# Performance work log

Hardware: AMD Instinct MI355X
Metric: run time of the kernel (lower is better)

## Reference

```python
import jax, jax.numpy as jnp
import numpy as np

DIM = 512
HEADS = 16
WS = 8          # window size
SHIFT = 4       # shift size
POSMLP = 32
MLP_HID = 4 * DIM
B = 32
HH = 56
WW = 56
EPS = 1e-5


def setup_inputs() -> dict:
    key = jax.random.key(0)
    ks = jax.random.split(key, 20)
    s = 0.02
    inp = {
        'x': jax.random.normal(ks[0], (B, HH * WW, DIM), jnp.float32),
        'g1': jnp.ones((DIM,), jnp.float32),
        'be1': jnp.zeros((DIM,), jnp.float32),
        'w_qkv': s * jax.random.normal(ks[1], (3 * DIM, DIM), jnp.float32),
        'b_qkv': jnp.zeros((3 * DIM,), jnp.float32),
        'pm_w1': s * jax.random.normal(ks[2], (POSMLP, 2), jnp.float32),
        'pm_b1': jnp.zeros((POSMLP,), jnp.float32),
        'pm_w2': s * jax.random.normal(ks[3], (HEADS, POSMLP), jnp.float32),
        'pm_b2': jnp.zeros((HEADS,), jnp.float32),
        'w_proj': s * jax.random.normal(ks[4], (DIM, DIM), jnp.float32),
        'b_proj': jnp.zeros((DIM,), jnp.float32),
        'g2': jnp.ones((DIM,), jnp.float32),
        'be2': jnp.zeros((DIM,), jnp.float32),
        'w_fc1': s * jax.random.normal(ks[5], (MLP_HID, DIM), jnp.float32),
        'b_fc1': jnp.zeros((MLP_HID,), jnp.float32),
        'w_fc2': s * jax.random.normal(ks[6], (DIM, MLP_HID), jnp.float32),
        'b_fc2': jnp.zeros((DIM,), jnp.float32),
        'H': HH,
        'W': WW,
    }
    return inp


def _layernorm(x, g, b):
    m = jnp.mean(x, -1, keepdims=True)
    v = jnp.mean(jnp.square(x - m), -1, keepdims=True)
    return (x - m) * jax.lax.rsqrt(v + EPS) * g + b


def _shift_mask(H, W, ws, sh):
    # static numpy construction of the (nW, N, N) 0/-100 shift mask
    img = np.zeros((H, W), np.float32)
    cnt = 0
    for hs in (slice(0, -ws), slice(-ws, -sh), slice(-sh, None)):
        for wsl in (slice(0, -ws), slice(-ws, -sh), slice(-sh, None)):
            img[hs, wsl] = cnt
            cnt += 1
    mw = img.reshape(H // ws, ws, W // ws, ws).transpose(0, 2, 1, 3).reshape(-1, ws * ws)
    diff = mw[:, None, :] - mw[:, :, None]
    return jnp.asarray(np.where(diff != 0, -100.0, 0.0).astype(np.float32))


def _pos_bias(ws, pm_w1, pm_b1, pm_w2, pm_b2):
    # log-CPB relative position bias computed by a tiny MLP -> (heads, N, N)
    g = jnp.stack(jnp.meshgrid(jnp.arange(ws), jnp.arange(ws), indexing='ij'))
    coords = g.reshape(2, -1).astype(jnp.float32)        # [2, N]
    d = coords[:, :, None] - coords[:, None, :]          # [2, N, N]
    d = jnp.sign(d) * jnp.log1p(jnp.abs(d))
    h = jax.nn.relu(jnp.einsum('cnm,oc->onm', d, pm_w1) + pm_b1[:, None, None])
    return jnp.einsum('onm,ho->hnm', h, pm_w2) + pm_b2[:, None, None]


def reference(x, g1, be1, w_qkv, b_qkv, pm_w1, pm_b1, pm_w2, pm_b2,
              w_proj, b_proj, g2, be2, w_fc1, b_fc1, w_fc2, b_fc2, H, W):
    ws, sh, nh = WS, SHIFT, HEADS
    Bb, L, C = x.shape
    hd = C // nh
    scale = hd ** -0.5
    N = ws * ws
    nWh, nWw = H // ws, W // ws
    nW = nWh * nWw

    shortcut = x
    xn = _layernorm(x, g1, be1).reshape(Bb, H, W, C)
    xn = jnp.roll(xn, (-sh, -sh), axis=(1, 2))
    # window partition -> (B*nW, N, C)
    xw = xn.reshape(Bb, nWh, ws, nWw, ws, C).transpose(0, 1, 3, 2, 4, 5).reshape(-1, N, C)

    qkv = (xw @ w_qkv.T + b_qkv).reshape(-1, N, 3, nh, hd).transpose(2, 0, 3, 1, 4)
    q, k, v = qkv[0], qkv[1], qkv[2]           # each (B*nW, nh, N, hd)

    attn = jnp.einsum('bhnd,bhmd->bhnm', q * scale, k)
    attn = attn + _pos_bias(ws, pm_w1, pm_b1, pm_w2, pm_b2)[None]

    mask = _shift_mask(H, W, ws, sh)           # (nW, N, N)
    attn = attn.reshape(Bb, nW, nh, N, N) + mask[None, :, None]
    attn = jax.nn.softmax(attn.reshape(-1, nh, N, N), axis=-1)

    out = jnp.einsum('bhnm,bhmd->bhnd', attn, v).transpose(0, 2, 1, 3).reshape(-1, N, C)
    out = out @ w_proj.T + b_proj

    # window reverse + roll back
    out = out.reshape(Bb, nWh, nWw, ws, ws, C).transpose(0, 1, 3, 2, 4, 5).reshape(Bb, H, W, C)
    out = jnp.roll(out, (sh, sh), axis=(1, 2)).reshape(Bb, L, C)

    x1 = shortcut + out
    h = jax.nn.gelu(_layernorm(x1, g2, be2) @ w_fc1.T + b_fc1, approximate=False)
    return x1 + (h @ w_fc2.T + b_fc2)
```

## Files before the change

kernel.cpp:

```cpp
#include <hip/hip_runtime.h>
#include <math.h>

typedef __bf16 bf16;
typedef bf16 bf16x8 __attribute__((ext_vector_type(8)));
typedef float f32x4 __attribute__((ext_vector_type(4)));

#define MFMA_BF16(a, b, c) __builtin_amdgcn_mfma_f32_16x16x32_bf16((a), (b), (c), 0, 0, 0)
#define GLDS16(gp, lp)                                                            \
  __builtin_amdgcn_global_load_lds((__attribute__((address_space(1))) void*)(gp), \
                                   (__attribute__((address_space(3))) void*)(lp), 16, 0, 0)
#define VMCNT(N) asm volatile("s_waitcnt vmcnt(" #N ")" ::: "memory")
#define LGKM(N) asm volatile("s_waitcnt lgkmcnt(" #N ")" ::: "memory")
#define SBAR __builtin_amdgcn_s_barrier()
#define SCHED0 __builtin_amdgcn_sched_barrier(0)

static constexpr int kDim   = 512;
static constexpr int kHeads = 16;
static constexpr int kHd    = 32;
static constexpr int kNt    = 64;
static constexpr int kNw    = 49;
static constexpr int kL     = 3136;
static constexpr int kToks  = 100352;
static constexpr int kWins  = 1568;
static constexpr int kHid   = 2048;
static constexpr size_t kQS = (size_t)kWins * kHeads * kNt * kHd;

__global__ __launch_bounds__(256) void wconv_kernel(const float* __restrict__ s,
                                                    bf16* __restrict__ d, int n8) {
  int i = blockIdx.x * 256 + threadIdx.x;
  if (i >= n8) return;
  const float4 a = *(const float4*)(s + i * 8);
  const float4 b = *(const float4*)(s + i * 8 + 4);
  bf16x8 o;
  o[0] = (bf16)a.x; o[1] = (bf16)a.y; o[2] = (bf16)a.z; o[3] = (bf16)a.w;
  o[4] = (bf16)b.x; o[5] = (bf16)b.y; o[6] = (bf16)b.z; o[7] = (bf16)b.w;
  *(bf16x8*)(d + i * 8) = o;
}

__global__ void posbias_kernel(const float* __restrict__ w1, const float* __restrict__ b1,
                               const float* __restrict__ w2, const float* __restrict__ b2,
                               float* __restrict__ tbl) {
  int idx = blockIdx.x * 256 + threadIdx.x;
  if (idx >= kHeads * kNt * kNt) return;
  int h = idx >> 12, n = (idx >> 6) & 63, m = idx & 63;
  float dr = (float)((n >> 3) - (m >> 3));
  float dc = (float)((n & 7) - (m & 7));
  dr = (dr > 0.f ? 1.f : (dr < 0.f ? -1.f : 0.f)) * log1pf(fabsf(dr));
  dc = (dc > 0.f ? 1.f : (dc < 0.f ? -1.f : 0.f)) * log1pf(fabsf(dc));
  float acc = b2[h];
  for (int o = 0; o < 32; ++o) {
    float hv = w1[o * 2] * dr + w1[o * 2 + 1] * dc + b1[o];
    acc += w2[h * 32 + o] * fmaxf(hv, 0.f);
  }
  tbl[idx] = acc;
}

template <int MODE>
__global__ __launch_bounds__(256) void ln_kernel(const float* __restrict__ x,
                                                 const float* __restrict__ g,
                                                 const float* __restrict__ be,
                                                 bf16* __restrict__ o) {
  const int t = blockIdx.x * 4 + (threadIdx.x >> 6);
  const int lane = threadIdx.x & 63;
  size_t src;
  if (MODE == 0) {
    const int win = t >> 6, n = t & 63;
    const int b = win / kNw, wi = win % kNw;
    const int h0 = ((wi / 7) * 8 + (n >> 3) + 4) % 56;
    const int w0 = ((wi % 7) * 8 + (n & 7) + 4) % 56;
    src = ((size_t)b * kL + h0 * 56 + w0) * kDim;
  } else {
    src = (size_t)t * kDim;
  }
  const float4 a = *(const float4*)(x + src + lane * 8);
  const float4 bq = *(const float4*)(x + src + lane * 8 + 4);
  float xf[8] = {a.x, a.y, a.z, a.w, bq.x, bq.y, bq.z, bq.w};
  float s = 0.f, s2 = 0.f;
#pragma unroll
  for (int j = 0; j < 8; ++j) { s += xf[j]; s2 += xf[j] * xf[j]; }
#pragma unroll
  for (int off = 32; off > 0; off >>= 1) { s += __shfl_xor(s, off); s2 += __shfl_xor(s2, off); }
  const float mean = s * (1.f / 512.f);
  const float rstd = rsqrtf(s2 * (1.f / 512.f) - mean * mean + 1e-5f);
  const float4 ga = *(const float4*)(g + lane * 8);
  const float4 gb = *(const float4*)(g + lane * 8 + 4);
  const float4 ba = *(const float4*)(be + lane * 8);
  const float4 bb = *(const float4*)(be + lane * 8 + 4);
  const float gv[8] = {ga.x, ga.y, ga.z, ga.w, gb.x, gb.y, gb.z, gb.w};
  const float bv[8] = {ba.x, ba.y, ba.z, ba.w, bb.x, bb.y, bb.z, bb.w};
  bf16x8 ov;
#pragma unroll
  for (int j = 0; j < 8; ++j) ov[j] = (bf16)((xf[j] - mean) * rstd * gv[j] + bv[j]);
  *(bf16x8*)(o + (size_t)t * kDim + lane * 8) = ov;
}

#define LOAD_A(dst, CB, KH, MB)                                        \
  _Pragma("unroll") for (int i = 0; i < 4; ++i)                        \
      dst[i] = *(const bf16x8*)(&L[CB][0][KH][aoff + (MB + i) * 512]);
#define LOAD_B(dst, CB, KH)                                            \
  _Pragma("unroll") for (int i = 0; i < 4; ++i)                        \
      dst[i] = *(const bf16x8*)(&L[CB][1][KH][boff + i * 512]);
#define MFMAS(MB, AF, BF)                                              \
  SCHED0;                                                              \
  __builtin_amdgcn_s_setprio(1);                                       \
  _Pragma("unroll") for (int mi = 0; mi < 4; ++mi)                     \
  _Pragma("unroll") for (int ni = 0; ni < 4; ++ni)                     \
      acc[MB + mi][ni] = MFMA_BF16(AF[mi], BF[ni], acc[MB + mi][ni]);  \
  __builtin_amdgcn_s_setprio(0)

template <int EPI>
__global__ __launch_bounds__(512, 2) void gemm256(const bf16* __restrict__ A, const bf16* __restrict__ B,
                                                  const float* __restrict__ bias, void* __restrict__ Cv,
                                                  const float* __restrict__ extra, int N, int K) {
  __shared__ __align__(16) bf16 L[2][2][2][8192];
  const int nbn = N >> 8;
  const int nwg = (int)gridDim.x;
  int wg = (int)blockIdx.x;
  {
    const int q = nwg >> 3, r = nwg & 7;
    const int xcd = wg & 7, loc = wg >> 3;
    wg = (xcd < r ? xcd * (q + 1) : r * (q + 1) + (xcd - r) * q) + loc;
  }
  const int bm = wg / nbn, bn = wg % nbn;
  const int tid = (int)threadIdx.x;
  const int wave = tid >> 6, lane = tid & 63;
  const int wm2 = wave >> 2, wn4 = wave & 3;
  const int quad = lane >> 4, l16 = lane & 15;

  const int sl0 = tid, sl1 = 512 + tid;
  const int rp0 = sl0 >> 3, ls0 = (sl0 & 7) ^ (rp0 & 7);
  const int rp1 = sl1 >> 3, ls1 = (sl1 & 7) ^ (rp1 & 7);
  const int row0 = rp0 * 2 + (ls0 >> 2), c0 = ls0 & 3;
  const int row1 = rp1 * 2 + (ls1 >> 2), c1 = ls1 & 3;
  const bf16* pa0 = A + (size_t)(bm * 256 + row0) * K + c0 * 8;
  const bf16* pa1 = A + (size_t)(bm * 256 + row1) * K + c1 * 8;
  const bf16* pb0 = B + (size_t)(bn * 256 + row0) * K + c0 * 8;
  const bf16* pb1 = B + (size_t)(bn * 256 + row1) * K + c1 * 8;

  const int ar = wm2 * 128 + l16, arp = ar >> 1;
  const int aoff = (arp * 8 + ((((ar & 1) << 2) | quad) ^ (arp & 7))) * 8;
  const int br = wn4 * 64 + l16, brp = br >> 1;
  const int boff = (brp * 8 + ((((br & 1) << 2) | quad) ^ (brp & 7))) * 8;

  f32x4 acc[8][4] = {};
  bf16x8 af0[4], af1[4], bfr0[4], bfr1[4];

  GLDS16(pa0, &L[0][0][0][sl0 * 8]);
  GLDS16(pa1, &L[0][0][0][sl1 * 8]);
  GLDS16(pb0, &L[0][1][0][sl0 * 8]);
  GLDS16(pb1, &L[0][1][0][sl1 * 8]);
  GLDS16(pa0 + 32, &L[0][0][1][sl0 * 8]);
  GLDS16(pa1 + 32, &L[0][0][1][sl1 * 8]);
  GLDS16(pb0 + 32, &L[0][1][1][sl0 * 8]);
  GLDS16(pb1 + 32, &L[0][1][1][sl1 * 8]);
  VMCNT(4);
  SBAR;
  LOAD_A(af0, 0, 0, 0);
  LOAD_B(bfr0, 0, 0);

#pragma unroll 2
  for (int kt = 0; kt < K; kt += 64) {
    const int cb = (kt >> 6) & 1, nb = cb ^ 1;
    const int kn = (kt + 64 < K) ? (kt + 64) : kt;
    LOAD_A(af1, cb, 0, 4);
    GLDS16(pa0 + kn, &L[nb][0][0][sl0 * 8]);
    GLDS16(pa1 + kn, &L[nb][0][0][sl1 * 8]);
    LGKM(4);
    MFMAS(0, af0, bfr0);
    VMCNT(2);
    SBAR;
    LOAD_A(af0, cb, 1, 0);
    LOAD_B(bfr1, cb, 1);
    GLDS16(pb0 + kn, &L[nb][1][0][sl0 * 8]);
    GLDS16(pb1 + kn, &L[nb][1][0][sl1 * 8]);
    LGKM(8);
    MFMAS(4, af1, bfr0);
    SBAR;
    LOAD_A(af1, cb, 1, 4);
    GLDS16(pa0 + kn + 32, &L[nb][0][1][sl0 * 8]);
    GLDS16(pa1 + kn + 32, &L[nb][0][1][sl1 * 8]);
    LGKM(4);
    MFMAS(0, af0, bfr1);
    VMCNT(2);
    SBAR;
    LOAD_A(af0, nb, 0, 0);
    LOAD_B(bfr0, nb, 0);
    GLDS16(pb0 + kn + 32, &L[nb][1][1][sl0 * 8]);
    GLDS16(pb1 + kn + 32, &L[nb][1][1][sl1 * 8]);
    LGKM(8);
    MFMAS(4, af1, bfr1);
    SBAR;
  }

  bf16* Cb = (bf16*)Cv;
  float* Cf = (float*)Cv;
#pragma unroll
  for (int mi = 0; mi < 8; ++mi) {
#pragma unroll
    for (int ni = 0; ni < 4; ++ni) {
      const int col = bn * 256 + wn4 * 64 + ni * 16 + l16;
      const float bb = bias[col];
#pragma unroll
      for (int r = 0; r < 4; ++r) {
        const int row = bm * 256 + wm2 * 128 + mi * 16 + quad * 4 + r;
        float val = acc[mi][ni][r] + bb;
        if constexpr (EPI == 1) {
          const int which = col >> 9, head = (col >> 5) & 15, d = col & 31;
          const int win = row >> 6, n = row & 63;
          Cb[(size_t)which * kQS + (((size_t)win * kHeads + head) * kNt + n) * kHd + d] = (bf16)val;
        } else if constexpr (EPI == 2) {
          val = 0.5f * val * (1.f + erff(val * 0.70710678118654752f));
          Cb[(size_t)row * N + col] = (bf16)val;
        } else if constexpr (EPI == 3) {
          Cf[(size_t)row * N + col] = val + extra[(size_t)row * N + col];
        } else {
          const int win = row >> 6, n = row & 63;
          const int b = win / kNw, wi = win % kNw;
          const int h0 = ((wi / 7) * 8 + (n >> 3) + 4) % 56;
          const int w0 = ((wi % 7) * 8 + (n & 7) + 4) % 56;
          const size_t dst = ((size_t)b * kL + h0 * 56 + w0) * kDim + col;
          Cf[dst] = val + extra[dst];
        }
      }
    }
  }
}

__device__ __forceinline__ int reg3(int x) { return x < 48 ? 0 : (x < 52 ? 1 : 2); }

__global__ __launch_bounds__(128) void attn_kernel(const bf16* __restrict__ qkv,
                                                   const float* __restrict__ ptbl,
                                                   bf16* __restrict__ out) {
  __shared__ float Sb[2][64 * 65];
  __shared__ float Rs[2][64];
  __shared__ bf16  Pb[2][64 * 72];
  __shared__ bf16  Vt[2][32 * 72];
  const int w = threadIdx.x >> 6, lane = threadIdx.x & 63;
  const int gwh = blockIdx.x * 2 + w;
  const int win = gwh >> 4, h = gwh & 15;
  const int quad = lane >> 4, l16 = lane & 15;
  const bf16* q = qkv + ((size_t)win * kHeads + h) * (kNt * kHd);
  const bf16* k = q + kQS;
  const bf16* v = q + 2 * kQS;

#pragma unroll
  for (int i = 0; i < 4; ++i) {
    const int row = i * 16 + (lane >> 2);
    const int d0 = (lane & 3) * 8;
    bf16x8 vv = *(const bf16x8*)(v + row * kHd + d0);
#pragma unroll
    for (int j = 0; j < 8; ++j) Vt[w][(d0 + j) * 72 + row] = vv[j];
  }

  bf16x8 qf[4], kf[4];
#pragma unroll
  for (int i = 0; i < 4; ++i) qf[i] = *(const bf16x8*)(q + (i * 16 + l16) * kHd + quad * 8);
#pragma unroll
  for (int j = 0; j < 4; ++j) kf[j] = *(const bf16x8*)(k + (j * 16 + l16) * kHd + quad * 8);
  f32x4 sa[4][4] = {};
#pragma unroll
  for (int i = 0; i < 4; ++i)
#pragma unroll
    for (int j = 0; j < 4; ++j) sa[i][j] = MFMA_BF16(qf[i], kf[j], sa[i][j]);

  const int wi = win % kNw;
  const int hb = (wi / 7) * 8, wb = (wi % 7) * 8;
  const float* bh = ptbl + h * 4096;
#pragma unroll
  for (int i = 0; i < 4; ++i) {
#pragma unroll
    for (int j = 0; j < 4; ++j) {
      const int ct = j * 16 + l16;
      const int crg = reg3(hb + (ct >> 3)) * 3 + reg3(wb + (ct & 7));
#pragma unroll
      for (int r = 0; r < 4; ++r) {
        const int rt = i * 16 + quad * 4 + r;
        const int rrg = reg3(hb + (rt >> 3)) * 3 + reg3(wb + (rt & 7));
        float sv = sa[i][j][r] * 0.17677669529663687f + bh[rt * 64 + ct];
        if (rrg != crg) sv -= 100.f;
        Sb[w][rt * 65 + ct] = sv;
      }
    }
  }
  __syncthreads();

  float mx = -1e30f;
  for (int i = 0; i < 64; ++i) mx = fmaxf(mx, Sb[w][lane * 65 + i]);
  float sum = 0.f;
  for (int i = 0; i < 64; ++i) {
    const float p = __expf(Sb[w][lane * 65 + i] - mx);
    sum += p;
    Pb[w][lane * 72 + i] = (bf16)p;
  }
  Rs[w][lane] = 1.f / sum;
  __syncthreads();

  f32x4 oa[4][2] = {};
#pragma unroll
  for (int kk = 0; kk < 2; ++kk) {
    bf16x8 pf[4], vf[2];
#pragma unroll
    for (int mi = 0; mi < 4; ++mi)
      pf[mi] = *(const bf16x8*)(&Pb[w][(mi * 16 + l16) * 72 + kk * 32 + quad * 8]);
#pragma unroll
    for (int nj = 0; nj < 2; ++nj)
      vf[nj] = *(const bf16x8*)(&Vt[w][(nj * 16 + l16) * 72 + kk * 32 + quad * 8]);
#pragma unroll
    for (int mi = 0; mi < 4; ++mi)
#pragma unroll
      for (int nj = 0; nj < 2; ++nj) oa[mi][nj] = MFMA_BF16(pf[mi], vf[nj], oa[mi][nj]);
  }
#pragma unroll
  for (int mi = 0; mi < 4; ++mi)
#pragma unroll
    for (int nj = 0; nj < 2; ++nj)
#pragma unroll
      for (int r = 0; r < 4; ++r) {
        const int row = mi * 16 + quad * 4 + r;
        const int col = nj * 16 + l16;
        out[((size_t)win * kNt + row) * kDim + h * kHd + col] = (bf16)(oa[mi][nj][r] * Rs[w][row]);
      }
}

extern "C" void kernel_launch(void* const* d_in, const int* in_sizes, int n_in,
                              void* d_out, int out_size, void* d_ws, size_t ws_size,
                              hipStream_t stream) {
  (void)in_sizes; (void)n_in; (void)out_size; (void)ws_size;
  const float* x      = (const float*)d_in[0];
  const float* g1     = (const float*)d_in[1];
  const float* be1    = (const float*)d_in[2];
  const float* w_qkv  = (const float*)d_in[3];
  const float* b_qkv  = (const float*)d_in[4];
  const float* pm_w1  = (const float*)d_in[5];
  const float* pm_b1  = (const float*)d_in[6];
  const float* pm_w2  = (const float*)d_in[7];
  const float* pm_b2  = (const float*)d_in[8];
  const float* w_proj = (const float*)d_in[9];
  const float* b_proj = (const float*)d_in[10];
  const float* g2     = (const float*)d_in[11];
  const float* be2    = (const float*)d_in[12];
  const float* w_fc1  = (const float*)d_in[13];
  const float* b_fc1  = (const float*)d_in[14];
  const float* w_fc2  = (const float*)d_in[15];
  const float* b_fc2  = (const float*)d_in[16];
  float* out = (float*)d_out;
  char* ws = (char*)d_ws;

  constexpr size_t OFF_WB   = 1u << 20;
  constexpr size_t OFF_XW   = OFF_WB + (8u << 20);
  constexpr size_t SZ_ACT   = (size_t)kToks * kDim * 2;
  constexpr size_t OFF_QKV  = OFF_XW + SZ_ACT;
  float* biastbl = (float*)ws;
  bf16* wqb = (bf16*)(ws + OFF_WB);
  bf16* wpb = wqb + 786432;
  bf16* w1b = wpb + 262144;
  bf16* w2b = w1b + 1048576;
  bf16* xw    = (bf16*)(ws + OFF_XW);
  bf16* attnb = xw;
  bf16* xn2   = xw;
  bf16* qkvb = (bf16*)(ws + OFF_QKV);
  float* x1  = (float*)(ws + OFF_QKV);
  bf16* hbuf = (bf16*)(ws + OFF_QKV + (size_t)kToks * kDim * 4);

  wconv_kernel<<<dim3(786432 / 2048), dim3(256), 0, stream>>>(w_qkv, wqb, 786432 / 8);
  wconv_kernel<<<dim3(262144 / 2048), dim3(256), 0, stream>>>(w_proj, wpb, 262144 / 8);
  wconv_kernel<<<dim3(1048576 / 2048), dim3(256), 0, stream>>>(w_fc1, w1b, 1048576 / 8);
  wconv_kernel<<<dim3(1048576 / 2048), dim3(256), 0, stream>>>(w_fc2, w2b, 1048576 / 8);
  posbias_kernel<<<dim3(256), dim3(256), 0, stream>>>(pm_w1, pm_b1, pm_w2, pm_b2, biastbl);
  ln_kernel<0><<<dim3(kToks / 4), dim3(256), 0, stream>>>(x, g1, be1, xw);
  gemm256<1><<<dim3((kToks / 256) * (1536 / 256)), dim3(512), 0, stream>>>(
      xw, wqb, b_qkv, qkvb, nullptr, 1536, 512);
  attn_kernel<<<dim3(kWins * kHeads / 2), dim3(128), 0, stream>>>(qkvb, biastbl, attnb);
  gemm256<4><<<dim3((kToks / 256) * (512 / 256)), dim3(512), 0, stream>>>(
      attnb, wpb, b_proj, x1, x, 512, 512);
  ln_kernel<1><<<dim3(kToks / 4), dim3(256), 0, stream>>>(x1, g2, be2, xn2);
  constexpr int kChunk = kToks / 4;
  for (int c = 0; c < 4; ++c) {
    const size_t ro = (size_t)c * kChunk * kDim;
    gemm256<2><<<dim3((kChunk / 256) * (kHid / 256)), dim3(512), 0, stream>>>(
        xn2 + ro, w1b, b_fc1, hbuf, nullptr, kHid, 512);
    gemm256<3><<<dim3((kChunk / 256) * (512 / 256)), dim3(512), 0, stream>>>(
        hbuf, w2b, b_fc2, out + ro, x1 + ro, 512, kHid);
  }
}
```

Before: 1.683 ms.

## Swap MFMA operands for row-contiguous accumulators and peel last K iteration

The MFMA A/B operands are swapped, so each lane's four accumulator values run along consecutive output columns instead of consecutive rows. The epilogue can then issue vectorized 4-wide stores and residual loads (bf16x4 and float4) instead of scalar ones, for every epilogue variant. The last K iteration is peeled out of the main loop, which removes the redundant prefetch of the final tile. Changing the register-to-output mapping risks mis-indexing, and the peeled tail adds code size.

New measurement: 1.674 ms. About the same (-0.6%).

```diff
diff --git a/kernel.cpp b/kernel.cpp
--- a/kernel.cpp
+++ b/kernel.cpp
@@ -2,6 +2,7 @@
 #include <math.h>
 
 typedef __bf16 bf16;
+typedef bf16 bf16x4 __attribute__((ext_vector_type(4)));
 typedef bf16 bf16x8 __attribute__((ext_vector_type(8)));
 typedef float f32x4 __attribute__((ext_vector_type(4)));
 
@@ -105,7 +106,7 @@
   __builtin_amdgcn_s_setprio(1);                                       \
   _Pragma("unroll") for (int mi = 0; mi < 4; ++mi)                     \
   _Pragma("unroll") for (int ni = 0; ni < 4; ++ni)                     \
-      acc[MB + mi][ni] = MFMA_BF16(AF[mi], BF[ni], acc[MB + mi][ni]);  \
+      acc[MB + mi][ni] = MFMA_BF16(BF[ni], AF[mi], acc[MB + mi][ni]);  \
   __builtin_amdgcn_s_setprio(0)
 
 template <int EPI>
@@ -159,9 +160,9 @@
   LOAD_B(bfr0, 0, 0);
 
 #pragma unroll 2
-  for (int kt = 0; kt < K; kt += 64) {
+  for (int kt = 0; kt < K - 64; kt += 64) {
     const int cb = (kt >> 6) & 1, nb = cb ^ 1;
-    const int kn = (kt + 64 < K) ? (kt + 64) : kt;
+    const int kn = kt + 64;
     LOAD_A(af1, cb, 0, 4);
     GLDS16(pa0 + kn, &L[nb][0][0][sl0 * 8]);
     GLDS16(pa1 + kn, &L[nb][0][0][sl1 * 8]);
@@ -191,36 +192,67 @@
     MFMAS(4, af1, bfr1);
     SBAR;
   }
+  {
+    const int cb = ((K >> 6) - 1) & 1;
+    LOAD_A(af1, cb, 0, 4);
+    LGKM(4);
+    MFMAS(0, af0, bfr0);
+    VMCNT(0);
+    SBAR;
+    LOAD_A(af0, cb, 1, 0);
+    LOAD_B(bfr1, cb, 1);
+    LGKM(8);
+    MFMAS(4, af1, bfr0);
+    SBAR;
+    LOAD_A(af1, cb, 1, 4);
+    LGKM(4);
+    MFMAS(0, af0, bfr1);
+    SBAR;
+    LGKM(0);
+    MFMAS(4, af1, bfr1);
+  }
 
   bf16* Cb = (bf16*)Cv;
   float* Cf = (float*)Cv;
 #pragma unroll
   for (int mi = 0; mi < 8; ++mi) {
+    const int row = bm * 256 + wm2 * 128 + mi * 16 + l16;
 #pragma unroll
     for (int ni = 0; ni < 4; ++ni) {
-      const int col = bn * 256 + wn4 * 64 + ni * 16 + l16;
-      const float bb = bias[col];
-#pragma unroll
-      for (int r = 0; r < 4; ++r) {
-        const int row = bm * 256 + wm2 * 128 + mi * 16 + quad * 4 + r;
-        float val = acc[mi][ni][r] + bb;
-        if constexpr (EPI == 1) {
-          const int which = col >> 9, head = (col >> 5) & 15, d = col & 31;
-          const int win = row >> 6, n = row & 63;
-          Cb[(size_t)which * kQS + (((size_t)win * kHeads + head) * kNt + n) * kHd + d] = (bf16)val;
-        } else if constexpr (EPI == 2) {
-          val = 0.5f * val * (1.f + erff(val * 0.70710678118654752f));
-          Cb[(size_t)row * N + col] = (bf16)val;
-        } else if constexpr (EPI == 3) {
-          Cf[(size_t)row * N + col] = val + extra[(size_t)row * N + col];
-        } else {
-          const int win = row >> 6, n = row & 63;
-          const int b = win / kNw, wi = win % kNw;
-          const int h0 = ((wi / 7) * 8 + (n >> 3) + 4) % 56;
-          const int w0 = ((wi % 7) * 8 + (n & 7) + 4) % 56;
-          const size_t dst = ((size_t)b * kL + h0 * 56 + w0) * kDim + col;
-          Cf[dst] = val + extra[dst];
+      const int colb = bn * 256 + wn4 * 64 + ni * 16 + quad * 4;
+      const float4 bq = *(const float4*)(bias + colb);
+      const float bbv[4] = {bq.x, bq.y, bq.z, bq.w};
+      float v4[4];
+#pragma unroll
+      for (int r = 0; r < 4; ++r) v4[r] = acc[mi][ni][r] + bbv[r];
+      if constexpr (EPI == 1) {
+        const int which = colb >> 9, head = (colb >> 5) & 15, d = colb & 31;
+        const int win = row >> 6, n = row & 63;
+        bf16x4 ov;
+#pragma unroll
+        for (int r = 0; r < 4; ++r) ov[r] = (bf16)v4[r];
+        *(bf16x4*)(Cb + (size_t)which * kQS + (((size_t)win * kHeads + head) * kNt + n) * kHd + d) = ov;
+      } else if constexpr (EPI == 2) {
+        bf16x4 ov;
+#pragma unroll
+        for (int r = 0; r < 4; ++r) {
+          const float g = 0.5f * v4[r] * (1.f + erff(v4[r] * 0.70710678118654752f));
+          ov[r] = (bf16)g;
         }
+        *(bf16x4*)(Cb + (size_t)row * N + colb) = ov;
+      } else if constexpr (EPI == 3) {
+        const float4 ex = *(const float4*)(extra + (size_t)row * N + colb);
+        float4 o4 = {v4[0] + ex.x, v4[1] + ex.y, v4[2] + ex.z, v4[3] + ex.w};
+        *(float4*)(Cf + (size_t)row * N + colb) = o4;
+      } else {
+        const int win = row >> 6, n = row & 63;
+        const int b = win / kNw, wi = win % kNw;
+        const int h0 = ((wi / 7) * 8 + (n >> 3) + 4) % 56;
+        const int w0 = ((wi % 7) * 8 + (n & 7) + 4) % 56;
+        const size_t dst = ((size_t)b * kL + h0 * 56 + w0) * kDim + colb;
+        const float4 ex = *(const float4*)(extra + dst);
+        float4 o4 = {v4[0] + ex.x, v4[1] + ex.y, v4[2] + ex.z, v4[3] + ex.w};
+        *(float4*)(Cf + dst) = o4;
       }
     }
   }
```
